# Optimization experiments

Hardware: AMD Instinct MI355X
Metric: run time of the kernel (lower is better)

## Reference

```python
import jax, jax.numpy as jnp
import numpy as np

B, T, C = 8, 2048, 1024
HS, HO = 64, 64  # head_size, head_output_dim

def setup_inputs() -> dict:
    key = jax.random.key(0)
    k1, k2, k3, k4 = jax.random.split(key, 4)
    x = jax.random.normal(k1, (B, T, C), dtype=jnp.float32)
    Wk = jax.random.normal(k2, (HS, C), dtype=jnp.float32) * (C ** -0.5)
    Wq = jax.random.normal(k3, (HS, C), dtype=jnp.float32) * (C ** -0.5)
    Wv = jax.random.normal(k4, (HO, C), dtype=jnp.float32) * (C ** -0.5)
    return {"x": x, "Wk": Wk, "Wq": Wq, "Wv": Wv}

def reference(x, Wk, Wq, Wv):
    Bx, Tx, Cx = x.shape
    k = jnp.einsum('btc,hc->bth', x, Wk)  # [B,T,HS]
    q = jnp.einsum('btc,hc->bth', x, Wq)  # [B,T,HS]
    v = jnp.einsum('btc,oc->bto', x, Wv)  # [B,T,HO]
    scores = jnp.einsum('bth,bsh->bts', q, k)  # [B,T,T]
    causal = jnp.tril(jnp.ones((Tx, Tx), dtype=bool))
    scores = jnp.where(causal, scores, -jnp.inf)
    # original scales AFTER masking; -inf * scale stays -inf, same softmax result
    weights = jax.nn.softmax(scores * (HS ** -0.5), axis=-1)
    return jnp.einsum('bts,bso->bto', weights, v)
```

## Files before the change

kernel.cpp:

```cpp
#include <hip/hip_runtime.h>
#include <hip/hip_bf16.h>

typedef __attribute__((ext_vector_type(8))) short short8;
typedef __attribute__((ext_vector_type(4))) float float4v;

#define LOG2E 1.44269504088896340736f

__device__ __forceinline__ unsigned short f2bf(float f) {
    unsigned int u = __float_as_uint(f);
    unsigned int r = (u + 0x7fffu + ((u >> 16) & 1u)) >> 16;
    return (unsigned short)r;
}

__global__ void wconv_kernel(const float* __restrict__ Wk, const float* __restrict__ Wq,
                             const float* __restrict__ Wv, unsigned short* __restrict__ Wb) {
    int i = blockIdx.x * 256 + threadIdx.x;
    if (i >= 192 * 1024) return;
    float v;
    if (i < 65536)       v = Wk[i];
    else if (i < 131072) v = Wq[i - 65536];
    else                 v = Wv[i - 131072];
    Wb[i] = f2bf(v);
}

__global__ __launch_bounds__(256) void proj_kernel(
    const float* __restrict__ x, const unsigned short* __restrict__ Wb,
    unsigned short* __restrict__ qs, unsigned short* __restrict__ ks,
    unsigned short* __restrict__ vT) {
    __shared__ unsigned short Bl[2][12288];
    __shared__ unsigned short Al[2][2048];

    const int tid  = threadIdx.x;
    const int lane = tid & 63;
    const int wave = tid >> 6;
    const int rg   = wave & 1;
    const int g    = wave >> 1;
    const int quad = lane >> 4;
    const int l16  = lane & 15;
    const int t0   = blockIdx.x * 32;

    const int brow_in = lane >> 3;
    const int bchunk  = lane & 7;
    const int bwchunk = bchunk ^ brow_in;

    const int ar = tid >> 3;
    const int ak = tid & 7;
    const float* xsrc = x + (size_t)(t0 + ar) * 1024 + ak * 8;
    const int awoff = ar * 64 + ((ak ^ (ar & 7)) * 8);

    const int arow = rg * 16 + l16;
    const int swz  = l16 & 7;

    float4v acc[6];
#pragma unroll
    for (int n = 0; n < 6; n++) acc[n] = (float4v){0.f, 0.f, 0.f, 0.f};

#define STAGE_LOAD_B(REG, KN)                                                     \
    {                                                                             \
        _Pragma("unroll")                                                         \
        for (int i = 0; i < 6; i++) {                                             \
            const int rowg = (wave * 6 + i) * 8 + brow_in;                        \
            REG[i] = *(const short8*)(Wb + (size_t)rowg * 1024 + (KN) + bchunk * 8); \
        }                                                                         \
    }

#define STAGE_WRITE_B(BUF, REG)                                                   \
    {                                                                             \
        _Pragma("unroll")                                                         \
        for (int i = 0; i < 6; i++)                                               \
            *(short8*)&Bl[BUF][(wave * 6 + i) * 512 + brow_in * 64 + bwchunk * 8] = REG[i]; \
    }

#define LOAD_A_G(F0, F1, KN)                              \
    {                                                     \
        F0 = *(const float4v*)(xsrc + (KN));              \
        F1 = *(const float4v*)(xsrc + (KN) + 4);          \
    }

#define STAGE_WRITE_A(BUF, F0, F1)                        \
    {                                                     \
        short8 w;                                         \
        _Pragma("unroll")                                 \
        for (int j = 0; j < 4; j++) {                     \
            w[j]     = (short)f2bf(F0[j]);                \
            w[4 + j] = (short)f2bf(F1[j]);                \
        }                                                 \
        *(short8*)&Al[BUF][awoff] = w;                    \
    }

    short8 breg[6];
    float4v aS[2][2];
    float4v a0f0, a0f1;
    STAGE_LOAD_B(breg, 0)
    asm volatile("" ::: "memory");
    LOAD_A_G(a0f0, a0f1, 0)
    asm volatile("" ::: "memory");
    LOAD_A_G(aS[1][0], aS[1][1], 64)
    asm volatile("s_waitcnt vmcnt(2)" ::: "memory");
    STAGE_WRITE_B(0, breg)
    STAGE_WRITE_A(0, a0f0, a0f1)
    asm volatile("s_waitcnt lgkmcnt(0)" ::: "memory");
    __builtin_amdgcn_s_barrier();

#pragma unroll
    for (int kt = 0; kt < 16; kt++) {
        __builtin_amdgcn_sched_barrier(0);
        if (kt < 15) {
            STAGE_LOAD_B(breg, (kt + 1) * 64)
        }
        asm volatile("" ::: "memory");
        if (kt < 14) {
            LOAD_A_G(aS[kt & 1][0], aS[kt & 1][1], (kt + 2) * 64)
        }
        asm volatile("" ::: "memory");

        const unsigned short* Bc = Bl[kt & 1];
        const unsigned short* Ac = Al[kt & 1];
#pragma unroll
        for (int kc = 0; kc < 2; kc++) {
            const int coff = ((kc * 4 + quad) ^ swz) * 8;
            const short8 af = *(const short8*)&Ac[arow * 64 + coff];
#pragma unroll
            for (int n = 0; n < 6; n++) {
                const int row = (g * 6 + n) * 16 + l16;
                const short8 bf = *(const short8*)&Bc[row * 64 + coff];
                acc[n] = __builtin_amdgcn_mfma_f32_16x16x32_bf16(af, bf, acc[n], 0, 0, 0);
            }
        }

        if (kt < 15) {
            if (kt < 14) {
                asm volatile("s_waitcnt vmcnt(2)" ::: "memory");
            } else {
                asm volatile("s_waitcnt vmcnt(0)" ::: "memory");
            }
            STAGE_WRITE_B((kt + 1) & 1, breg)
            STAGE_WRITE_A((kt + 1) & 1, aS[(kt + 1) & 1][0], aS[(kt + 1) & 1][1])
            asm volatile("s_waitcnt lgkmcnt(0)" ::: "memory");
            __builtin_amdgcn_s_barrier();
        }
    }
#undef STAGE_LOAD_B
#undef STAGE_WRITE_B
#undef LOAD_A_G
#undef STAGE_WRITE_A

    const int rowD = t0 + rg * 16 + quad * 4;
#pragma unroll
    for (int r = 0; r < 4; r++) {
        const int t = rowD + r;
        const int b = t >> 11, tt = t & 2047;
        if (g == 0) {
#pragma unroll
            for (int n = 0; n < 4; n++)
                ks[(size_t)t * 64 + n * 16 + l16] = f2bf(acc[n][r]);
#pragma unroll
            for (int n = 4; n < 6; n++)
                qs[(size_t)t * 64 + (n - 4) * 16 + l16] = f2bf(acc[n][r] * 0.125f);
        } else {
#pragma unroll
            for (int n = 0; n < 2; n++)
                qs[(size_t)t * 64 + (n + 2) * 16 + l16] = f2bf(acc[n][r] * 0.125f);
#pragma unroll
            for (int n = 2; n < 6; n++)
                vT[(size_t)b * 131072 + (size_t)((n - 2) * 16 + l16) * 2048 + tt] = f2bf(acc[n][r]);
        }
    }
}

__global__ __launch_bounds__(256) void attn_kernel(
    const unsigned short* __restrict__ qs, const unsigned short* __restrict__ ks,
    const unsigned short* __restrict__ vT, float* __restrict__ out) {
    __shared__ unsigned short Kl[4 * 64 * 72];
    __shared__ unsigned short Vl[64 * 264];
    __shared__ unsigned short P[4][16 * 72];
    __shared__ float Ll[4][16];
    float* Of = (float*)Kl;

    const int tid  = threadIdx.x;
    const int lane = tid & 63;
    const int wave = tid >> 6;
    const int quad = lane >> 4;
    const int l16  = lane & 15;
    const int bx   = blockIdx.x;
    const int b    = bx & 7;
    const int i    = bx >> 3;
    const int qt   = (i & 1) ? (127 - (i >> 1)) : (i >> 1);
    const int t0   = qt * 16;

    const unsigned short* qb = qs + (size_t)b * 131072;
    const unsigned short* kb = ks + (size_t)b * 131072;
    const unsigned short* vb = vT + (size_t)b * 131072;

    const int ksr = tid >> 3;
    const int ksc = (tid & 7) * 8;
    const int vsr = tid >> 5;
    const int vsc = (tid & 31) * 8;

    const int qrow = t0 + l16;
    const short8 qf0 = *(const short8*)(qb + (size_t)qrow * 64 + quad * 8);
    const short8 qf1 = *(const short8*)(qb + (size_t)qrow * 64 + 32 + quad * 8);

    float4v o[4];
#pragma unroll
    for (int ot = 0; ot < 4; ot++) o[ot] = (float4v){0.f, 0.f, 0.f, 0.f};
    float lpart = 0.f;

    const int nkb  = (qt >> 2) + 1;
    const int nsup = (nkb + 3) >> 2;

    for (int s = 0; s < nsup; s++) {
        const int key0 = s * 256;
        __syncthreads();
#pragma unroll
        for (int i2 = 0; i2 < 8; i2++) {
            int kr = key0 + i2 * 32 + ksr; kr = kr < 2047 ? kr : 2047;
            *(short8*)&Kl[(i2 * 32 + ksr) * 72 + ksc] = *(const short8*)(kb + (size_t)kr * 64 + ksc);
        }
#pragma unroll
        for (int i2 = 0; i2 < 8; i2++) {
            const int orow = i2 * 8 + vsr;
            int kc2 = key0 + vsc; kc2 = kc2 < 2040 ? kc2 : 2040;
            *(short8*)&Vl[orow * 264 + vsc] = *(const short8*)(vb + (size_t)orow * 2048 + kc2);
        }
        __syncthreads();

        const int jt = s * 4 + wave;
        if (jt < nkb) {
            const int kbase = wave * 64;
            float4v sv[4];
#pragma unroll
            for (int kt = 0; kt < 4; kt++) {
                const short8 ka = *(const short8*)&Kl[(kbase + kt * 16 + l16) * 72 + quad * 8];
                const short8 kc = *(const short8*)&Kl[(kbase + kt * 16 + l16) * 72 + 32 + quad * 8];
                float4v z = (float4v){0.f, 0.f, 0.f, 0.f};
                z = __builtin_amdgcn_mfma_f32_16x16x32_bf16(ka, qf0, z, 0, 0, 0);
                sv[kt] = __builtin_amdgcn_mfma_f32_16x16x32_bf16(kc, qf1, z, 0, 0, 0);
            }
            if (jt == nkb - 1) {
#pragma unroll
                for (int kt = 0; kt < 4; kt++)
#pragma unroll
                    for (int r = 0; r < 4; r++)
                        if (jt * 64 + kt * 16 + quad * 4 + r > qrow) sv[kt][r] = -1e30f;
            }
#pragma unroll
            for (int kt = 0; kt < 4; kt++) {
                float p0 = exp2f(sv[kt][0] * LOG2E);
                float p1 = exp2f(sv[kt][1] * LOG2E);
                float p2 = exp2f(sv[kt][2] * LOG2E);
                float p3 = exp2f(sv[kt][3] * LOG2E);
                lpart += (p0 + p1) + (p2 + p3);
                unsigned int lo = (unsigned int)f2bf(p0) | ((unsigned int)f2bf(p1) << 16);
                unsigned int hi = (unsigned int)f2bf(p2) | ((unsigned int)f2bf(p3) << 16);
                unsigned long long w = ((unsigned long long)hi << 32) | lo;
                *(unsigned long long*)&P[wave][l16 * 72 + kt * 16 + quad * 4] = w;
            }
#pragma unroll
            for (int kc = 0; kc < 2; kc++) {
                const short8 pf = *(const short8*)&P[wave][l16 * 72 + kc * 32 + quad * 8];
#pragma unroll
                for (int ot = 0; ot < 4; ot++) {
                    const short8 vf = *(const short8*)&Vl[(ot * 16 + l16) * 264 + wave * 64 + kc * 32 + quad * 8];
                    o[ot] = __builtin_amdgcn_mfma_f32_16x16x32_bf16(pf, vf, o[ot], 0, 0, 0);
                }
            }
        }
    }

    lpart += __shfl_xor(lpart, 16);
    lpart += __shfl_xor(lpart, 32);
    __syncthreads();
#pragma unroll
    for (int r = 0; r < 4; r++)
#pragma unroll
        for (int ot = 0; ot < 4; ot++)
            Of[wave * 1088 + (quad * 4 + r) * 68 + ot * 16 + l16] = o[ot][r];
    if (lane < 16) Ll[wave][lane] = lpart;
    __syncthreads();

    {
        const int row = tid >> 4;
        const int c0  = (tid & 15) * 4;
        const float lsum = Ll[0][row] + Ll[1][row] + Ll[2][row] + Ll[3][row];
        float4v v0 = *(const float4v*)&Of[0 * 1088 + row * 68 + c0];
        float4v v1 = *(const float4v*)&Of[1 * 1088 + row * 68 + c0];
        float4v v2 = *(const float4v*)&Of[2 * 1088 + row * 68 + c0];
        float4v v3 = *(const float4v*)&Of[3 * 1088 + row * 68 + c0];
        float4v res;
        const float inv = 1.0f / lsum;
#pragma unroll
        for (int j = 0; j < 4; j++)
            res[j] = ((v0[j] + v1[j]) + (v2[j] + v3[j])) * inv;
        float* ob = out + (size_t)b * 131072 + (size_t)(t0 + row) * 64 + c0;
        *(float4v*)ob = res;
    }
}

extern "C" void kernel_launch(void* const* d_in, const int* in_sizes, int n_in,
                              void* d_out, int out_size, void* d_ws, size_t ws_size,
                              hipStream_t stream) {
    const float* x  = (const float*)d_in[0];
    const float* Wk = (const float*)d_in[1];
    const float* Wq = (const float*)d_in[2];
    const float* Wv = (const float*)d_in[3];
    float* out = (float*)d_out;

    unsigned short* Wb  = (unsigned short*)d_ws;
    unsigned short* qsb = (unsigned short*)((char*)d_ws + 393216);
    unsigned short* ksb = qsb + 1048576;
    unsigned short* vTb = ksb + 1048576;

    hipLaunchKernelGGL(wconv_kernel, dim3(768), dim3(256), 0, stream, Wk, Wq, Wv, Wb);
    hipLaunchKernelGGL(proj_kernel, dim3(512), dim3(256), 0, stream, x, Wb, qsb, ksb, vTb);
    hipLaunchKernelGGL(attn_kernel, dim3(1024), dim3(256), 0, stream, qsb, ksb, vTb, out);
}
```

Measured before the change: 142.4 us.

## Process 32 query rows per attention block, splitting waves by query half and key half

```diff
diff --git a/kernel.cpp b/kernel.cpp
--- a/kernel.cpp
+++ b/kernel.cpp
@@ -185,8 +185,11 @@
     const int bx   = blockIdx.x;
     const int b    = bx & 7;
     const int i    = bx >> 3;
-    const int qt   = (i & 1) ? (127 - (i >> 1)) : (i >> 1);
-    const int t0   = qt * 16;
+    const int qt   = (i & 1) ? (63 - (i >> 1)) : (i >> 1);
+    const int t0   = qt * 32;
+
+    const int qsub  = wave & 1;
+    const int khalf = wave >> 1;
 
     const unsigned short* qb = qs + (size_t)b * 131072;
     const unsigned short* kb = ks + (size_t)b * 131072;
@@ -197,7 +200,7 @@
     const int vsr = tid >> 5;
     const int vsc = (tid & 31) * 8;
 
-    const int qrow = t0 + l16;
+    const int qrow = t0 + qsub * 16 + l16;
     const short8 qf0 = *(const short8*)(qb + (size_t)qrow * 64 + quad * 8);
     const short8 qf1 = *(const short8*)(qb + (size_t)qrow * 64 + 32 + quad * 8);
 
@@ -206,8 +209,9 @@
     for (int ot = 0; ot < 4; ot++) o[ot] = (float4v){0.f, 0.f, 0.f, 0.f};
     float lpart = 0.f;
 
-    const int nkb  = (qt >> 2) + 1;
-    const int nsup = (nkb + 3) >> 2;
+    const int nkb   = (qt >> 1) + 1;
+    const int nkb_w = ((2 * qt + qsub) >> 2) + 1;
+    const int nsup  = (nkb + 3) >> 2;
 
     for (int s = 0; s < nsup; s++) {
         const int key0 = s * 256;
@@ -225,44 +229,47 @@
         }
         __syncthreads();
 
-        const int jt = s * 4 + wave;
-        if (jt < nkb) {
-            const int kbase = wave * 64;
-            float4v sv[4];
-#pragma unroll
-            for (int kt = 0; kt < 4; kt++) {
-                const short8 ka = *(const short8*)&Kl[(kbase + kt * 16 + l16) * 72 + quad * 8];
-                const short8 kc = *(const short8*)&Kl[(kbase + kt * 16 + l16) * 72 + 32 + quad * 8];
-                float4v z = (float4v){0.f, 0.f, 0.f, 0.f};
-                z = __builtin_amdgcn_mfma_f32_16x16x32_bf16(ka, qf0, z, 0, 0, 0);
-                sv[kt] = __builtin_amdgcn_mfma_f32_16x16x32_bf16(kc, qf1, z, 0, 0, 0);
-            }
-            if (jt == nkb - 1) {
-#pragma unroll
-                for (int kt = 0; kt < 4; kt++)
-#pragma unroll
-                    for (int r = 0; r < 4; r++)
-                        if (jt * 64 + kt * 16 + quad * 4 + r > qrow) sv[kt][r] = -1e30f;
-            }
-#pragma unroll
-            for (int kt = 0; kt < 4; kt++) {
-                float p0 = exp2f(sv[kt][0] * LOG2E);
-                float p1 = exp2f(sv[kt][1] * LOG2E);
-                float p2 = exp2f(sv[kt][2] * LOG2E);
-                float p3 = exp2f(sv[kt][3] * LOG2E);
-                lpart += (p0 + p1) + (p2 + p3);
-                unsigned int lo = (unsigned int)f2bf(p0) | ((unsigned int)f2bf(p1) << 16);
-                unsigned int hi = (unsigned int)f2bf(p2) | ((unsigned int)f2bf(p3) << 16);
-                unsigned long long w = ((unsigned long long)hi << 32) | lo;
-                *(unsigned long long*)&P[wave][l16 * 72 + kt * 16 + quad * 4] = w;
-            }
-#pragma unroll
-            for (int kc = 0; kc < 2; kc++) {
-                const short8 pf = *(const short8*)&P[wave][l16 * 72 + kc * 32 + quad * 8];
-#pragma unroll
-                for (int ot = 0; ot < 4; ot++) {
-                    const short8 vf = *(const short8*)&Vl[(ot * 16 + l16) * 264 + wave * 64 + kc * 32 + quad * 8];
-                    o[ot] = __builtin_amdgcn_mfma_f32_16x16x32_bf16(pf, vf, o[ot], 0, 0, 0);
+#pragma unroll
+        for (int kk = 0; kk < 2; kk++) {
+            const int jt = s * 4 + khalf * 2 + kk;
+            if (jt < nkb_w) {
+                const int kbase = (khalf * 2 + kk) * 64;
+                float4v sv[4];
+#pragma unroll
+                for (int kt = 0; kt < 4; kt++) {
+                    const short8 ka = *(const short8*)&Kl[(kbase + kt * 16 + l16) * 72 + quad * 8];
+                    const short8 kc = *(const short8*)&Kl[(kbase + kt * 16 + l16) * 72 + 32 + quad * 8];
+                    float4v z = (float4v){0.f, 0.f, 0.f, 0.f};
+                    z = __builtin_amdgcn_mfma_f32_16x16x32_bf16(ka, qf0, z, 0, 0, 0);
+                    sv[kt] = __builtin_amdgcn_mfma_f32_16x16x32_bf16(kc, qf1, z, 0, 0, 0);
+                }
+                if (jt == nkb_w - 1) {
+#pragma unroll
+                    for (int kt = 0; kt < 4; kt++)
+#pragma unroll
+                        for (int r = 0; r < 4; r++)
+                            if (jt * 64 + kt * 16 + quad * 4 + r > qrow) sv[kt][r] = -1e30f;
+                }
+#pragma unroll
+                for (int kt = 0; kt < 4; kt++) {
+                    float p0 = exp2f(sv[kt][0] * LOG2E);
+                    float p1 = exp2f(sv[kt][1] * LOG2E);
+                    float p2 = exp2f(sv[kt][2] * LOG2E);
+                    float p3 = exp2f(sv[kt][3] * LOG2E);
+                    lpart += (p0 + p1) + (p2 + p3);
+                    unsigned int lo = (unsigned int)f2bf(p0) | ((unsigned int)f2bf(p1) << 16);
+                    unsigned int hi = (unsigned int)f2bf(p2) | ((unsigned int)f2bf(p3) << 16);
+                    unsigned long long w = ((unsigned long long)hi << 32) | lo;
+                    *(unsigned long long*)&P[wave][l16 * 72 + kt * 16 + quad * 4] = w;
+                }
+#pragma unroll
+                for (int kc = 0; kc < 2; kc++) {
+                    const short8 pf = *(const short8*)&P[wave][l16 * 72 + kc * 32 + quad * 8];
+#pragma unroll
+                    for (int ot = 0; ot < 4; ot++) {
+                        const short8 vf = *(const short8*)&Vl[(ot * 16 + l16) * 264 + kbase + kc * 32 + quad * 8];
+                        o[ot] = __builtin_amdgcn_mfma_f32_16x16x32_bf16(pf, vf, o[ot], 0, 0, 0);
+                    }
                 }
             }
         }
@@ -282,18 +289,19 @@
     {
         const int row = tid >> 4;
         const int c0  = (tid & 15) * 4;
-        const float lsum = Ll[0][row] + Ll[1][row] + Ll[2][row] + Ll[3][row];
-        float4v v0 = *(const float4v*)&Of[0 * 1088 + row * 68 + c0];
-        float4v v1 = *(const float4v*)&Of[1 * 1088 + row * 68 + c0];
-        float4v v2 = *(const float4v*)&Of[2 * 1088 + row * 68 + c0];
-        float4v v3 = *(const float4v*)&Of[3 * 1088 + row * 68 + c0];
-        float4v res;
-        const float inv = 1.0f / lsum;
-#pragma unroll
-        for (int j = 0; j < 4; j++)
-            res[j] = ((v0[j] + v1[j]) + (v2[j] + v3[j])) * inv;
-        float* ob = out + (size_t)b * 131072 + (size_t)(t0 + row) * 64 + c0;
-        *(float4v*)ob = res;
+#pragma unroll
+        for (int q2 = 0; q2 < 2; q2++) {
+            const float lsum = Ll[q2][row] + Ll[q2 + 2][row];
+            float4v v0 = *(const float4v*)&Of[q2 * 1088 + row * 68 + c0];
+            float4v v1 = *(const float4v*)&Of[(q2 + 2) * 1088 + row * 68 + c0];
+            float4v res;
+            const float inv = 1.0f / lsum;
+#pragma unroll
+            for (int j = 0; j < 4; j++)
+                res[j] = (v0[j] + v1[j]) * inv;
+            float* ob = out + (size_t)b * 131072 + (size_t)(t0 + q2 * 16 + row) * 64 + c0;
+            *(float4v*)ob = res;
+        }
     }
 }
 
@@ -313,5 +321,5 @@
 
     hipLaunchKernelGGL(wconv_kernel, dim3(768), dim3(256), 0, stream, Wk, Wq, Wv, Wb);
     hipLaunchKernelGGL(proj_kernel, dim3(512), dim3(256), 0, stream, x, Wb, qsb, ksb, vTb);
-    hipLaunchKernelGGL(attn_kernel, dim3(1024), dim3(256), 0, stream, qsb, ksb, vTb, out);
-}
+    hipLaunchKernelGGL(attn_kernel, dim3(512), dim3(256), 0, stream, qsb, ksb, vTb, out);
+}
```

Measured after the change: 134.5 us. 1.06x faster.

## Assign 16 query rows per wave and share K/V tiles across waves

Applied to the files above, without the earlier changes.

```diff
diff --git a/kernel.cpp b/kernel.cpp
--- a/kernel.cpp
+++ b/kernel.cpp
@@ -174,8 +174,6 @@
     __shared__ unsigned short Kl[4 * 64 * 72];
     __shared__ unsigned short Vl[64 * 264];
     __shared__ unsigned short P[4][16 * 72];
-    __shared__ float Ll[4][16];
-    float* Of = (float*)Kl;
 
     const int tid  = threadIdx.x;
     const int lane = tid & 63;
@@ -184,9 +182,8 @@
     const int l16  = lane & 15;
     const int bx   = blockIdx.x;
     const int b    = bx & 7;
-    const int i    = bx >> 3;
-    const int qt   = (i & 1) ? (127 - (i >> 1)) : (i >> 1);
-    const int t0   = qt * 16;
+    const int qt   = bx >> 3;
+    const int t0   = qt * 64;
 
     const unsigned short* qb = qs + (size_t)b * 131072;
     const unsigned short* kb = ks + (size_t)b * 131072;
@@ -197,7 +194,7 @@
     const int vsr = tid >> 5;
     const int vsc = (tid & 31) * 8;
 
-    const int qrow = t0 + l16;
+    const int qrow = t0 + wave * 16 + l16;
     const short8 qf0 = *(const short8*)(qb + (size_t)qrow * 64 + quad * 8);
     const short8 qf1 = *(const short8*)(qb + (size_t)qrow * 64 + 32 + quad * 8);
 
@@ -206,7 +203,7 @@
     for (int ot = 0; ot < 4; ot++) o[ot] = (float4v){0.f, 0.f, 0.f, 0.f};
     float lpart = 0.f;
 
-    const int nkb  = (qt >> 2) + 1;
+    const int nkb  = qt + 1;
     const int nsup = (nkb + 3) >> 2;
 
     for (int s = 0; s < nsup; s++) {
@@ -225,44 +222,47 @@
         }
         __syncthreads();
 
-        const int jt = s * 4 + wave;
-        if (jt < nkb) {
-            const int kbase = wave * 64;
-            float4v sv[4];
-#pragma unroll
-            for (int kt = 0; kt < 4; kt++) {
-                const short8 ka = *(const short8*)&Kl[(kbase + kt * 16 + l16) * 72 + quad * 8];
-                const short8 kc = *(const short8*)&Kl[(kbase + kt * 16 + l16) * 72 + 32 + quad * 8];
-                float4v z = (float4v){0.f, 0.f, 0.f, 0.f};
-                z = __builtin_amdgcn_mfma_f32_16x16x32_bf16(ka, qf0, z, 0, 0, 0);
-                sv[kt] = __builtin_amdgcn_mfma_f32_16x16x32_bf16(kc, qf1, z, 0, 0, 0);
-            }
-            if (jt == nkb - 1) {
-#pragma unroll
-                for (int kt = 0; kt < 4; kt++)
-#pragma unroll
-                    for (int r = 0; r < 4; r++)
-                        if (jt * 64 + kt * 16 + quad * 4 + r > qrow) sv[kt][r] = -1e30f;
-            }
-#pragma unroll
-            for (int kt = 0; kt < 4; kt++) {
-                float p0 = exp2f(sv[kt][0] * LOG2E);
-                float p1 = exp2f(sv[kt][1] * LOG2E);
-                float p2 = exp2f(sv[kt][2] * LOG2E);
-                float p3 = exp2f(sv[kt][3] * LOG2E);
-                lpart += (p0 + p1) + (p2 + p3);
-                unsigned int lo = (unsigned int)f2bf(p0) | ((unsigned int)f2bf(p1) << 16);
-                unsigned int hi = (unsigned int)f2bf(p2) | ((unsigned int)f2bf(p3) << 16);
-                unsigned long long w = ((unsigned long long)hi << 32) | lo;
-                *(unsigned long long*)&P[wave][l16 * 72 + kt * 16 + quad * 4] = w;
-            }
-#pragma unroll
-            for (int kc = 0; kc < 2; kc++) {
-                const short8 pf = *(const short8*)&P[wave][l16 * 72 + kc * 32 + quad * 8];
-#pragma unroll
-                for (int ot = 0; ot < 4; ot++) {
-                    const short8 vf = *(const short8*)&Vl[(ot * 16 + l16) * 264 + wave * 64 + kc * 32 + quad * 8];
-                    o[ot] = __builtin_amdgcn_mfma_f32_16x16x32_bf16(pf, vf, o[ot], 0, 0, 0);
+#pragma unroll
+        for (int kk = 0; kk < 4; kk++) {
+            const int jt = s * 4 + kk;
+            if (jt < nkb) {
+                const int kbase = kk * 64;
+                float4v sv[4];
+#pragma unroll
+                for (int kt = 0; kt < 4; kt++) {
+                    const short8 ka = *(const short8*)&Kl[(kbase + kt * 16 + l16) * 72 + quad * 8];
+                    const short8 kc = *(const short8*)&Kl[(kbase + kt * 16 + l16) * 72 + 32 + quad * 8];
+                    float4v z = (float4v){0.f, 0.f, 0.f, 0.f};
+                    z = __builtin_amdgcn_mfma_f32_16x16x32_bf16(ka, qf0, z, 0, 0, 0);
+                    sv[kt] = __builtin_amdgcn_mfma_f32_16x16x32_bf16(kc, qf1, z, 0, 0, 0);
+                }
+                if (jt == nkb - 1) {
+#pragma unroll
+                    for (int kt = 0; kt < 4; kt++)
+#pragma unroll
+                        for (int r = 0; r < 4; r++)
+                            if (jt * 64 + kt * 16 + quad * 4 + r > qrow) sv[kt][r] = -1e30f;
+                }
+#pragma unroll
+                for (int kt = 0; kt < 4; kt++) {
+                    float p0 = exp2f(sv[kt][0] * LOG2E);
+                    float p1 = exp2f(sv[kt][1] * LOG2E);
+                    float p2 = exp2f(sv[kt][2] * LOG2E);
+                    float p3 = exp2f(sv[kt][3] * LOG2E);
+                    lpart += (p0 + p1) + (p2 + p3);
+                    unsigned int lo = (unsigned int)f2bf(p0) | ((unsigned int)f2bf(p1) << 16);
+                    unsigned int hi = (unsigned int)f2bf(p2) | ((unsigned int)f2bf(p3) << 16);
+                    unsigned long long w = ((unsigned long long)hi << 32) | lo;
+                    *(unsigned long long*)&P[wave][l16 * 72 + kt * 16 + quad * 4] = w;
+                }
+#pragma unroll
+                for (int kc = 0; kc < 2; kc++) {
+                    const short8 pf = *(const short8*)&P[wave][l16 * 72 + kc * 32 + quad * 8];
+#pragma unroll
+                    for (int ot = 0; ot < 4; ot++) {
+                        const short8 vf = *(const short8*)&Vl[(ot * 16 + l16) * 264 + kbase + kc * 32 + quad * 8];
+                        o[ot] = __builtin_amdgcn_mfma_f32_16x16x32_bf16(pf, vf, o[ot], 0, 0, 0);
+                    }
                 }
             }
         }
@@ -270,30 +270,14 @@
 
     lpart += __shfl_xor(lpart, 16);
     lpart += __shfl_xor(lpart, 32);
-    __syncthreads();
-#pragma unroll
-    for (int r = 0; r < 4; r++)
+
+    const int rowO = t0 + wave * 16 + quad * 4;
+#pragma unroll
+    for (int r = 0; r < 4; r++) {
+        const float inv = 1.0f / __shfl(lpart, quad * 4 + r);
 #pragma unroll
         for (int ot = 0; ot < 4; ot++)
-            Of[wave * 1088 + (quad * 4 + r) * 68 + ot * 16 + l16] = o[ot][r];
-    if (lane < 16) Ll[wave][lane] = lpart;
-    __syncthreads();
-
-    {
-        const int row = tid >> 4;
-        const int c0  = (tid & 15) * 4;
-        const float lsum = Ll[0][row] + Ll[1][row] + Ll[2][row] + Ll[3][row];
-        float4v v0 = *(const float4v*)&Of[0 * 1088 + row * 68 + c0];
-        float4v v1 = *(const float4v*)&Of[1 * 1088 + row * 68 + c0];
-        float4v v2 = *(const float4v*)&Of[2 * 1088 + row * 68 + c0];
-        float4v v3 = *(const float4v*)&Of[3 * 1088 + row * 68 + c0];
-        float4v res;
-        const float inv = 1.0f / lsum;
-#pragma unroll
-        for (int j = 0; j < 4; j++)
-            res[j] = ((v0[j] + v1[j]) + (v2[j] + v3[j])) * inv;
-        float* ob = out + (size_t)b * 131072 + (size_t)(t0 + row) * 64 + c0;
-        *(float4v*)ob = res;
+            out[(size_t)b * 131072 + (size_t)(rowO + r) * 64 + ot * 16 + l16] = o[ot][r] * inv;
     }
 }
 
@@ -313,5 +297,5 @@
 
     hipLaunchKernelGGL(wconv_kernel, dim3(768), dim3(256), 0, stream, Wk, Wq, Wv, Wb);
     hipLaunchKernelGGL(proj_kernel, dim3(512), dim3(256), 0, stream, x, Wb, qsb, ksb, vTb);
-    hipLaunchKernelGGL(attn_kernel, dim3(1024), dim3(256), 0, stream, qsb, ksb, vTb, out);
-}
+    hipLaunchKernelGGL(attn_kernel, dim3(256), dim3(256), 0, stream, qsb, ksb, vTb, out);
+}
```

After: 146.0 us. +2.5%, slower.
